# Kernel tuning notes

Hardware: AMD Instinct MI355X
Metric: run time of the kernel (lower is better)

## Reference

```python
import jax, jax.numpy as jnp
import numpy as np

PRIOR = 0.2
TEMP = 1.0
THRESHOLD = 0.5
B, L, D, H = 8, 4096, 768, 512


def setup_inputs() -> dict:
    key = jax.random.key(0)
    k1, k2, k3, k4 = jax.random.split(key, 4)
    hidden = jax.random.normal(k1, (B, L, D), jnp.float32)
    # MLP params: Linear(D,H) -> ReLU -> Linear(H,1)
    W1 = jax.random.normal(k2, (D, H), jnp.float32) / np.sqrt(D).astype(np.float32)
    b1 = jnp.zeros((H,), jnp.float32)
    W2 = jax.random.normal(k3, (H, 1), jnp.float32) / np.sqrt(H).astype(np.float32)
    b2 = jnp.zeros((1,), jnp.float32)
    # pre-sampled uniform noise for the RelaxedBernoulli logistic reparameterization
    noise_u = jax.random.uniform(k4, (B, L), jnp.float32, minval=1e-6, maxval=1.0 - 1e-6)
    return dict(hidden=hidden, W1=W1, b1=b1, W2=W2, b2=b2, noise_u=noise_u)


def reference(hidden, W1, b1, W2, b2, noise_u):
    bs, seq_len, model_dim = hidden.shape
    # boundary MLP -> per-token logits [B, L]
    h = jax.nn.relu(jnp.einsum('bld,dh->blh', hidden, W1) + b1)
    logits = (jnp.einsum('blh,ho->blo', h, W2) + b2)[..., 0]
    # RelaxedBernoulli rsample: sigmoid((logits + logistic_noise) / temp),
    # since logit(sigmoid(logits)) == logits
    logistic_noise = jnp.log(noise_u) - jnp.log1p(-noise_u)
    soft_boundaries = jax.nn.sigmoid((logits + logistic_noise) / TEMP)
    hard_bin = (soft_boundaries > THRESHOLD).astype(soft_boundaries.dtype)
    # straight-through estimator
    hard_boundaries = soft_boundaries + jax.lax.stop_gradient(hard_bin - soft_boundaries)
    # segment id of each token: number of boundaries strictly before it
    # (boundary token is the last element of its segment)
    seg = (jnp.cumsum(hard_bin, axis=1) - hard_bin).astype(jnp.int32)  # [B, L] in [0, L)
    ids = (seg + seq_len * jnp.arange(bs, dtype=jnp.int32)[:, None]).reshape(-1)
    flat = hidden.reshape(bs * seq_len, model_dim)
    seg_sum = jax.ops.segment_sum(flat, ids, num_segments=bs * seq_len)
    seg_cnt = jax.ops.segment_sum(jnp.ones((bs * seq_len,), hidden.dtype), ids,
                                  num_segments=bs * seq_len)
    # mean pooling per segment; unused segment slots stay zero (padded to L segments,
    # equivalent to the torch [S,B,D]->transpose output up to zero padding)
    pooled = (seg_sum / jnp.maximum(seg_cnt, 1.0)[:, None]).reshape(bs, seq_len, model_dim)
    # hinge loss on boundary rate: penalize |rate - (prior+0.05)| beyond margin 0.05
    ratio = jnp.mean(hard_boundaries)
    loss = jax.nn.relu(jnp.abs(ratio - (PRIOR + 0.05)) - 0.05)
    num_boundaries = jnp.sum(hard_bin)
    total_positions = jnp.asarray(bs * seq_len, jnp.float32)
    return pooled, loss, num_boundaries, total_positions
```

## Files before the change

kernel.cpp:

```cpp
#include <hip/hip_runtime.h>
#include <math.h>

typedef __attribute__((ext_vector_type(8))) short short8;
typedef __attribute__((ext_vector_type(4))) float float4v;
typedef unsigned int uint;

#define BATCH 8
#define SEQ   4096
#define DIM   768
#define HID   512
#define M_TOK (BATCH * SEQ)

static __device__ __forceinline__ short f2bf_rne(float x) {
    unsigned int u = __float_as_uint(x);
    unsigned int r = (u + 0x7FFFu + ((u >> 16) & 1u)) >> 16;
    return (short)r;
}
static __device__ __forceinline__ uint pack_bf2(float a, float b) {
    return __builtin_amdgcn_perm(__float_as_uint(b), __float_as_uint(a), 0x07060302u);
}
union FragU { uint u[4]; short8 s; };
static __device__ __forceinline__ void gl2lds16(const void* g, void* l) {
    __builtin_amdgcn_global_load_lds(
        (const __attribute__((address_space(1))) unsigned int*)g,
        (__attribute__((address_space(3))) unsigned int*)l, 16, 0, 0);
}

__global__ __launch_bounds__(256) void prep_kernel(const float* __restrict__ W1,
                                                   short* __restrict__ W1T) {
    __shared__ float t[64][65];
    const int bk = blockIdx.x % 12, bn = blockIdx.x / 12;
    const int k0 = bk * 64, n0 = bn * 64;
    const int tr = threadIdx.x >> 6, tc = threadIdx.x & 63;
#pragma unroll
    for (int i = 0; i < 16; i++) {
        int k = tr + i * 4;
        t[k][tc] = W1[(size_t)(k0 + k) * HID + n0 + tc];
    }
    __syncthreads();
#pragma unroll
    for (int i = 0; i < 16; i++) {
        int n = tr + i * 4;
        W1T[(size_t)(n0 + n) * DIM + k0 + tc] = f2bf_rne(t[tc][n]);
    }
}

#define AS_BYTES 8192
#define BS_BYTES 32768
__global__ __launch_bounds__(256, 2) void mlp_kernel(const float* __restrict__ A,
                                                     const short* __restrict__ BT,
                                                     const float* __restrict__ b1,
                                                     const float* __restrict__ W2,
                                                     float* __restrict__ logits) {
    __shared__ float4v smem[(AS_BYTES + BS_BYTES) / 16];
    char* Asb = (char*)smem;
    char* Bsb = (char*)smem + AS_BYTES;

    const int m0 = blockIdx.x * 64;
    const int tid = threadIdx.x, wave = tid >> 6, lane = tid & 63;
    const int quad = lane >> 4, r = lane & 15;

    int a_go[2], a_lds[2], b_go[8], b_lds[8];
#pragma unroll
    for (int j = 0; j < 2; j++) {
        int ia = wave * 2 + j;
        int row = ia * 8 + (lane >> 3);
        int c = (lane & 7) ^ (row & 7);
        a_go[j] = row * DIM + c * 4;
        a_lds[j] = ia * 1024;
    }
#pragma unroll
    for (int j = 0; j < 8; j++) {
        int ib = wave * 8 + j;
        int n = ib * 16 + (lane >> 2);
        int c = lane & 3;
        b_go[j] = n * DIM + c * 8;
        b_lds[j] = ib * 1024;
    }

    float4v acc[4][8] = {};
    const float* Abase = A + (size_t)m0 * DIM;

    for (int p = 0; p < 24; ++p) {
        const int k0 = p * 32;
#pragma unroll
        for (int j = 0; j < 2; j++) gl2lds16(Abase + a_go[j] + k0, Asb + a_lds[j]);
#pragma unroll
        for (int j = 0; j < 8; j++) gl2lds16(BT + b_go[j] + k0, Bsb + b_lds[j]);
        __syncthreads();

        short8 bfr[8];
#pragma unroll
        for (int nf = 0; nf < 8; nf++)
            bfr[nf] = *(const short8*)(Bsb + (wave * 128 + nf * 16 + r) * 64 + quad * 16);
#pragma unroll
        for (int mf = 0; mf < 4; mf++) {
            int row = mf * 16 + r;
            int e0 = (2 * quad) ^ (row & 7);
            float4v f0 = *(const float4v*)(Asb + row * 128 + e0 * 16);
            float4v f1 = *(const float4v*)(Asb + row * 128 + (e0 ^ 1) * 16);
            FragU af;
            af.u[0] = pack_bf2(f0[0], f0[1]);
            af.u[1] = pack_bf2(f0[2], f0[3]);
            af.u[2] = pack_bf2(f1[0], f1[1]);
            af.u[3] = pack_bf2(f1[2], f1[3]);
#pragma unroll
            for (int nf = 0; nf < 8; nf++)
                acc[mf][nf] = __builtin_amdgcn_mfma_f32_16x16x32_bf16(
                    af.s, bfr[nf], acc[mf][nf], 0, 0, 0);
        }
        __syncthreads();
    }

    float b1v[8], w2v[8];
#pragma unroll
    for (int nf = 0; nf < 8; nf++) {
        int gc = wave * 128 + nf * 16 + r;
        b1v[nf] = b1[gc];
        w2v[nf] = W2[gc];
    }
    float* red = (float*)Asb;
#pragma unroll
    for (int mf = 0; mf < 4; mf++)
#pragma unroll
        for (int v = 0; v < 4; v++) {
            float pp = 0.f;
#pragma unroll
            for (int nf = 0; nf < 8; nf++) {
                float hh = acc[mf][nf][v] + b1v[nf];
                hh = hh > 0.f ? hh : 0.f;
                pp += hh * w2v[nf];
            }
#pragma unroll
            for (int off = 1; off < 16; off <<= 1) pp += __shfl_xor(pp, off, 64);
            if (r == 0) red[wave * 64 + mf * 16 + quad * 4 + v] = pp;
        }
    __syncthreads();
    if (tid < 64) {
        float s = red[tid] + red[64 + tid] + red[128 + tid] + red[192 + tid];
        logits[m0 + tid] = s;
    }
}

__global__ __launch_bounds__(1024) void boundary_kernel(const float* __restrict__ logits,
                                                        const float* __restrict__ b2p,
                                                        const float* __restrict__ noise,
                                                        int* __restrict__ starts,
                                                        int* __restrict__ nseg,
                                                        int* __restrict__ nbcount) {
    const int b = blockIdx.x, tid = threadIdx.x;
    const int base = tid * 4;
    const float b2 = b2p[0];
    int h[4], c = 0;
#pragma unroll
    for (int j = 0; j < 4; j++) {
        int l = base + j;
        float u = noise[b * SEQ + l];
        float lg = logits[b * SEQ + l] + b2 + logf(u) - log1pf(-u);
        h[j] = (lg > 0.f) ? 1 : 0;
        c += h[j];
    }
    const int lane = tid & 63, wid = tid >> 6;
    int inc = c;
    for (int off = 1; off < 64; off <<= 1) {
        int t = __shfl_up(inc, off, 64);
        if (lane >= off) inc += t;
    }
    __shared__ int wtot[16], woff[16], extra[2];
    if (lane == 63) wtot[wid] = inc;
    if (tid == 1023) extra[0] = h[3];
    __syncthreads();
    if (tid == 0) {
        int s = 0;
        for (int i = 0; i < 16; i++) { woff[i] = s; s += wtot[i]; }
        extra[1] = s;
    }
    __syncthreads();
    int run = (inc - c) + woff[wid];
#pragma unroll
    for (int j = 0; j < 4; j++) {
        int l = base + j;
        if (h[j]) {
            run++;
            if (l < SEQ - 1) starts[b * (SEQ + 1) + run] = l + 1;
        }
    }
    if (tid == 0) {
        int total = extra[1];
        int ns = total + (extra[0] ? 0 : 1);
        starts[b * (SEQ + 1)] = 0;
        starts[b * (SEQ + 1) + ns] = SEQ;
        nseg[b] = ns;
        nbcount[b] = total;
    }
}

__global__ __launch_bounds__(256) void pool_kernel(const float* __restrict__ hidden,
                                                   const int* __restrict__ starts,
                                                   const int* __restrict__ nseg,
                                                   float* __restrict__ out) {
    const int wid = threadIdx.x >> 6, lane = threadIdx.x & 63;
    const int s = blockIdx.x * 4 + wid, b = blockIdx.y;
    float* orow = out + (size_t)(b * SEQ + s) * DIM;
    float4v a0 = {0.f, 0.f, 0.f, 0.f}, a1 = a0, a2 = a0;
    const int ns = nseg[b];
    if (s < ns) {
        const int st = starts[b * (SEQ + 1) + s];
        const int en = starts[b * (SEQ + 1) + s + 1];
        float4v c0 = a0, c1 = a0, c2 = a0;
        const float* hbase = hidden + (size_t)(b * SEQ) * DIM;
        int row = st;
        for (; row + 2 <= en; row += 2) {
            const float* h0 = hbase + (size_t)row * DIM;
            const float* h1 = h0 + DIM;
            a0 += *(const float4v*)(h0 + lane * 4);
            a1 += *(const float4v*)(h0 + (lane + 64) * 4);
            a2 += *(const float4v*)(h0 + (lane + 128) * 4);
            c0 += *(const float4v*)(h1 + lane * 4);
            c1 += *(const float4v*)(h1 + (lane + 64) * 4);
            c2 += *(const float4v*)(h1 + (lane + 128) * 4);
        }
        if (row < en) {
            const float* h0 = hbase + (size_t)row * DIM;
            a0 += *(const float4v*)(h0 + lane * 4);
            a1 += *(const float4v*)(h0 + (lane + 64) * 4);
            a2 += *(const float4v*)(h0 + (lane + 128) * 4);
        }
        a0 += c0; a1 += c1; a2 += c2;
        const float invc = 1.f / (float)(en - st);
        a0 *= invc; a1 *= invc; a2 *= invc;
    }
    __builtin_nontemporal_store(a0, (float4v*)(orow + lane * 4));
    __builtin_nontemporal_store(a1, (float4v*)(orow + (lane + 64) * 4));
    __builtin_nontemporal_store(a2, (float4v*)(orow + (lane + 128) * 4));
}

__global__ void finalize_kernel(const int* __restrict__ nbcount, float* __restrict__ tail) {
    int nb = 0;
    for (int i = 0; i < BATCH; i++) nb += nbcount[i];
    float ratio = (float)nb / (float)M_TOK;
    float d = fabsf(ratio - 0.25f) - 0.05f;
    tail[0] = d > 0.f ? d : 0.f;
    tail[1] = (float)nb;
    tail[2] = (float)M_TOK;
}

extern "C" void kernel_launch(void* const* d_in, const int* in_sizes, int n_in,
                              void* d_out, int out_size, void* d_ws, size_t ws_size,
                              hipStream_t stream) {
    const float* hidden = (const float*)d_in[0];
    const float* W1     = (const float*)d_in[1];
    const float* b1     = (const float*)d_in[2];
    const float* W2     = (const float*)d_in[3];
    const float* b2     = (const float*)d_in[4];
    const float* noise  = (const float*)d_in[5];

    char* ws = (char*)d_ws;
    short* W1T    = (short*)(ws);
    float* logits = (float*)(ws + 786432);
    int*   starts = (int*)(ws + 917504);
    int*   nseg   = (int*)(ws + 917504 + 131104);
    int*   nbcount = nseg + 8;
    float* out    = (float*)d_out;

    prep_kernel<<<96, 256, 0, stream>>>(W1, W1T);
    mlp_kernel<<<512, 256, 0, stream>>>(hidden, W1T, b1, W2, logits);
    boundary_kernel<<<BATCH, 1024, 0, stream>>>(logits, b2, noise, starts, nseg, nbcount);
    pool_kernel<<<dim3(SEQ / 4, BATCH), 256, 0, stream>>>(hidden, starts, nseg, out);
    finalize_kernel<<<1, 1, 0, stream>>>(nbcount, out + (size_t)M_TOK * DIM);
}
```

Baseline: 242.7 us.

## Double-buffer MLP GEMM LDS tiles and enlarge block to 128 rows

Restructures the MLP GEMM kernel so each block covers 128 tokens with 8 waves in a 2x4 layout, which halves how often each block reloads the W1 tiles. It adds a double-buffered LDS pipeline in which the next k-step's global-to-LDS loads are issued before the MFMAs on the current buffer, and it drops one of the two barriers per step. LDS data is now stored directly in fragment order, which replaces the old XOR swizzle. LDS use grows to 96KB of dynamic shared memory per block, so occupancy may fall. Correctness now depends on the single barrier at the end of each step, which still sits in the unchanged part of the loop.

```diff
diff --git a/kernel.cpp b/kernel.cpp
--- a/kernel.cpp
+++ b/kernel.cpp
@@ -45,60 +45,64 @@
     }
 }
 
-#define AS_BYTES 8192
-#define BS_BYTES 32768
-__global__ __launch_bounds__(256, 2) void mlp_kernel(const float* __restrict__ A,
+#define MLP_BM    128
+#define MLP_STEPS 24
+#define MLP_ABYTES 16384
+#define MLP_BBYTES 32768
+#define MLP_BUF   (MLP_ABYTES + MLP_BBYTES)
+#define MLP_LDS   (2 * MLP_BUF)
+
+__global__ __launch_bounds__(512, 2) void mlp_kernel(const float* __restrict__ A,
                                                      const short* __restrict__ BT,
                                                      const float* __restrict__ b1,
                                                      const float* __restrict__ W2,
                                                      float* __restrict__ logits) {
-    __shared__ float4v smem[(AS_BYTES + BS_BYTES) / 16];
-    char* Asb = (char*)smem;
-    char* Bsb = (char*)smem + AS_BYTES;
-
-    const int m0 = blockIdx.x * 64;
+    extern __shared__ char smem[];
     const int tid = threadIdx.x, wave = tid >> 6, lane = tid & 63;
-    const int quad = lane >> 4, r = lane & 15;
-
-    int a_go[2], a_lds[2], b_go[8], b_lds[8];
-#pragma unroll
-    for (int j = 0; j < 2; j++) {
-        int ia = wave * 2 + j;
-        int row = ia * 8 + (lane >> 3);
-        int c = (lane & 7) ^ (row & 7);
-        a_go[j] = row * DIM + c * 4;
-        a_lds[j] = ia * 1024;
-    }
-#pragma unroll
-    for (int j = 0; j < 8; j++) {
-        int ib = wave * 8 + j;
-        int n = ib * 16 + (lane >> 2);
-        int c = lane & 3;
-        b_go[j] = n * DIM + c * 8;
-        b_lds[j] = ib * 1024;
+    const int q = lane >> 4, r = lane & 15;
+    const int wr = wave >> 2, wc = wave & 3;
+    const int m0 = blockIdx.x * MLP_BM;
+
+    const float* aS0 = A + (size_t)(m0 + wave * 16 + r) * DIM + q * 8;
+    const float* aS1 = aS0 + 4;
+    const int aD0 = wave * 2048, aD1 = wave * 2048 + 1024;
+    const short* bS[4];
+    int bD[4];
+#pragma unroll
+    for (int j = 0; j < 4; j++) {
+        int h = wave * 4 + j;
+        bS[j] = BT + (size_t)(h * 16 + r) * DIM + q * 8;
+        bD[j] = MLP_ABYTES + h * 1024;
     }
 
     float4v acc[4][8] = {};
-    const float* Abase = A + (size_t)m0 * DIM;
-
-    for (int p = 0; p < 24; ++p) {
-        const int k0 = p * 32;
-#pragma unroll
-        for (int j = 0; j < 2; j++) gl2lds16(Abase + a_go[j] + k0, Asb + a_lds[j]);
-#pragma unroll
-        for (int j = 0; j < 8; j++) gl2lds16(BT + b_go[j] + k0, Bsb + b_lds[j]);
-        __syncthreads();
+
+    gl2lds16(aS0, smem + aD0);
+    gl2lds16(aS1, smem + aD1);
+#pragma unroll
+    for (int j = 0; j < 4; j++) gl2lds16(bS[j], smem + bD[j]);
+    __syncthreads();
+
+    for (int p = 0; p < MLP_STEPS; ++p) {
+        if (p + 1 < MLP_STEPS) {
+            char* nb = smem + ((p + 1) & 1) * MLP_BUF;
+            const int ko = (p + 1) * 32;
+            gl2lds16(aS0 + ko, nb + aD0);
+            gl2lds16(aS1 + ko, nb + aD1);
+#pragma unroll
+            for (int j = 0; j < 4; j++) gl2lds16(bS[j] + ko, nb + bD[j]);
+        }
+        char* base = smem + (p & 1) * MLP_BUF;
 
         short8 bfr[8];
 #pragma unroll
         for (int nf = 0; nf < 8; nf++)
-            bfr[nf] = *(const short8*)(Bsb + (wave * 128 + nf * 16 + r) * 64 + quad * 16);
+            bfr[nf] = *(const short8*)(base + MLP_ABYTES + (wc * 8 + nf) * 1024 + lane * 16);
 #pragma unroll
         for (int mf = 0; mf < 4; mf++) {
-            int row = mf * 16 + r;
-            int e0 = (2 * quad) ^ (row & 7);
-            float4v f0 = *(const float4v*)(Asb + row * 128 + e0 * 16);
-            float4v f1 = *(const float4v*)(Asb + row * 128 + (e0 ^ 1) * 16);
+            const int g = wr * 4 + mf;
+            float4v f0 = *(const float4v*)(base + g * 2048 + lane * 16);
+            float4v f1 = *(const float4v*)(base + g * 2048 + 1024 + lane * 16);
             FragU af;
             af.u[0] = pack_bf2(f0[0], f0[1]);
             af.u[1] = pack_bf2(f0[2], f0[3]);
@@ -115,11 +119,11 @@
     float b1v[8], w2v[8];
 #pragma unroll
     for (int nf = 0; nf < 8; nf++) {
-        int gc = wave * 128 + nf * 16 + r;
+        int gc = wc * 128 + nf * 16 + r;
         b1v[nf] = b1[gc];
         w2v[nf] = W2[gc];
     }
-    float* red = (float*)Asb;
+    float* red = (float*)smem;
 #pragma unroll
     for (int mf = 0; mf < 4; mf++)
 #pragma unroll
@@ -133,12 +137,11 @@
             }
 #pragma unroll
             for (int off = 1; off < 16; off <<= 1) pp += __shfl_xor(pp, off, 64);
-            if (r == 0) red[wave * 64 + mf * 16 + quad * 4 + v] = pp;
-        }
-    __syncthreads();
-    if (tid < 64) {
-        float s = red[tid] + red[64 + tid] + red[128 + tid] + red[192 + tid];
-        logits[m0 + tid] = s;
+            if (r == 0) red[wc * 128 + wr * 64 + mf * 16 + q * 4 + v] = pp;
+        }
+    __syncthreads();
+    if (tid < 128) {
+        logits[m0 + tid] = red[tid] + red[128 + tid] + red[256 + tid] + red[384 + tid];
     }
 }
 
@@ -263,8 +266,15 @@
     int*   nbcount = nseg + 8;
     float* out    = (float*)d_out;
 
+    static bool s_mlp_attr = false;
+    if (!s_mlp_attr) {
+        hipFuncSetAttribute(reinterpret_cast<const void*>(mlp_kernel),
+                            hipFuncAttributeMaxDynamicSharedMemorySize, MLP_LDS);
+        s_mlp_attr = true;
+    }
+
     prep_kernel<<<96, 256, 0, stream>>>(W1, W1T);
-    mlp_kernel<<<512, 256, 0, stream>>>(hidden, W1T, b1, W2, logits);
+    mlp_kernel<<<M_TOK / MLP_BM, 512, MLP_LDS, stream>>>(hidden, W1T, b1, W2, logits);
     boundary_kernel<<<BATCH, 1024, 0, stream>>>(logits, b2, noise, starts, nseg, nbcount);
     pool_kernel<<<dim3(SEQ / 4, BATCH), 256, 0, stream>>>(hidden, starts, nseg, out);
     finalize_kernel<<<1, 1, 0, stream>>>(nbcount, out + (size_t)M_TOK * DIM);
```

Result: no change. 246.0 us (+1.4%).
